# Kernel optimization log

Hardware: AMD Instinct MI355X
Metric: run time of the kernel (lower is better)

The kernel has to match this reference:

```python
import jax, jax.numpy as jnp
import numpy as np

TOP_K = 8


def setup_inputs() -> dict:
    key = jax.random.key(0)
    ks = jax.random.split(key, 7)
    B, D, E = 65536, 1024, 64
    return {
        "x": jax.random.normal(ks[0], (B, D), dtype=jnp.float32),
        "Wg": jax.random.normal(ks[1], (E, D), dtype=jnp.float32) * 0.02,
        "bg": jax.random.normal(ks[2], (E,), dtype=jnp.float32) * 0.02,
        "Wn": jax.random.normal(ks[3], (E, D), dtype=jnp.float32) * 0.02,
        "bn": jax.random.normal(ks[4], (E,), dtype=jnp.float32) * 0.02,
        "We": jax.random.normal(ks[5], (E, D), dtype=jnp.float32) * 0.02,
        "noise": jax.random.normal(ks[6], (B, E), dtype=jnp.float32),
    }


def reference(x, Wg, bg, Wn, bn, We, noise):
    # Router (faithful to original: top-k is taken on noise_logits,
    # and noisy_logits is computed but does not affect the output).
    logits = x @ Wg.T + bg                      # [B, E]
    noise_logits = x @ Wn.T + bn                # [B, E]
    noisy_logits = logits + noise * jax.nn.softplus(noise_logits)  # unused downstream
    del noisy_logits

    top_vals, top_idx = jax.lax.top_k(noise_logits, TOP_K)  # [B, K]
    B, E = noise_logits.shape
    neg_inf = jnp.array(-jnp.inf, dtype=x.dtype)
    sparse_logits = jnp.full((B, E), neg_inf, dtype=x.dtype)
    sparse_logits = sparse_logits.at[jnp.arange(B)[:, None], top_idx].set(top_vals)
    routing_weights = jax.nn.softmax(sparse_logits, axis=-1)  # [B, E]

    # All experts are Linear(d, 1, bias=False): stack into one GEMM.
    expert_out = x @ We.T                        # [B, E]
    final_out = jnp.sum(expert_out * routing_weights, axis=-1, keepdims=True)  # [B, 1]
    return final_out
```

## Files before the change

kernel.cpp:

```cpp
#include <hip/hip_runtime.h>

#define DDIM 1024
#define NEXP 64
#define TOPK 8
#define BK 32
#define ROWS 64
#define NTILE 32
#define TAUF 5.0e-3f
#define TAUB 1.0e-2f

typedef __attribute__((ext_vector_type(8))) short short8;
typedef __attribute__((ext_vector_type(4))) float f32x4;

static __device__ __forceinline__ unsigned int f2u(float f) { return __builtin_bit_cast(unsigned int, f); }
static __device__ __forceinline__ float u2f(unsigned int u) { return __builtin_bit_cast(float, u); }

static __device__ __forceinline__ unsigned short bf_hi_rne(float x) {
    unsigned int u = f2u(x);
    return (unsigned short)((u + (0x7FFFu + ((u >> 16) & 1u))) >> 16);
}

static __device__ __forceinline__ void split2(float x, unsigned short& h, unsigned short& l) {
    unsigned int u = f2u(x);
    unsigned int uh = (u + (0x7FFFu + ((u >> 16) & 1u))) & 0xFFFF0000u;
    h = (unsigned short)(uh >> 16);
    float rem = x - u2f(uh);
    l = (unsigned short)(f2u(rem) >> 16);
}

__global__ __launch_bounds__(256) void conv_w_kernel(
    const float* __restrict__ Wn, const float* __restrict__ We, char* __restrict__ wsW)
{
    int g = blockIdx.x * 256 + threadIdx.x;
    int e = g >> 7, c128 = g & 127;
    int k = c128 << 3;
    int t = k >> 5, c = (k >> 3) & 3;
    const float* np = Wn + (size_t)e * DDIM + k;
    const float* ep = We + (size_t)e * DDIM + k;
    f32x4 n0 = ((const f32x4*)np)[0], n1 = ((const f32x4*)np)[1];
    f32x4 e0 = ((const f32x4*)ep)[0], e1 = ((const f32x4*)ep)[1];
    short8 nh, nl, eh;
#pragma unroll
    for (int i = 0; i < 4; i++) { unsigned short h, l; split2(n0[i], h, l); nh[i] = (short)h; nl[i] = (short)l; }
#pragma unroll
    for (int i = 0; i < 4; i++) { unsigned short h, l; split2(n1[i], h, l); nh[i + 4] = (short)h; nl[i + 4] = (short)l; }
#pragma unroll
    for (int i = 0; i < 4; i++) eh[i] = (short)bf_hi_rne(e0[i]);
#pragma unroll
    for (int i = 0; i < 4; i++) eh[i + 4] = (short)bf_hi_rne(e1[i]);
    size_t dst = (size_t)t * 12288 + (size_t)(e >> 4) * 3072 + (size_t)((c * 16 + (e & 15)) * 16);
    *(short8*)(wsW + dst)        = nh;
    *(short8*)(wsW + dst + 1024) = nl;
    *(short8*)(wsW + dst + 2048) = eh;
}

template <int PRE>
__global__ __launch_bounds__(256, 4) void moe_kernel(
    const float* __restrict__ x, const float* __restrict__ Wn,
    const float* __restrict__ bn, const float* __restrict__ We,
    const char* __restrict__ wsW, float* __restrict__ out)
{
    __shared__ __align__(16) char smem[33792];

    const int tid = threadIdx.x;
    const int wid = tid >> 6;
    const int lane = tid & 63;
    const int fr = lane & 15;
    const int fq = lane >> 4;
    const int blockRow = blockIdx.x * ROWS;

    const int srow = tid >> 2, sg = tid & 3;
    const int swz = (srow * 64 + sg * 16) ^ ((srow & 7) << 4);
    const float* xsrc = x + (size_t)(blockRow + srow) * DDIM + sg * 8;

    f32x4 sxA0, sxA1, sxB0, sxB1, sxC0, sxC1;
    short8 whA, wlA, ehA, whB, wlB, ehB, whC, wlC, ehC;

    const char* wbase = wsW + wid * 3072 + lane * 16;

#define XLOAD_A(t) { const float* p = xsrc + (t) * BK; sxA0 = ((const f32x4*)p)[0]; sxA1 = ((const f32x4*)p)[1]; }
#define XLOAD_B(t) { const float* p = xsrc + (t) * BK; sxB0 = ((const f32x4*)p)[0]; sxB1 = ((const f32x4*)p)[1]; }
#define XLOAD_C(t) { const float* p = xsrc + (t) * BK; sxC0 = ((const f32x4*)p)[0]; sxC1 = ((const f32x4*)p)[1]; }

#define WLOAD(t, wh, wl, eh) { \
    if constexpr (PRE) { \
        const char* wp = wbase + (size_t)(t) * 12288; \
        wh = *(const short8*)(wp); \
        wl = *(const short8*)(wp + 1024); \
        eh = *(const short8*)(wp + 2048); \
    } else { \
        const float* np_ = Wn + (size_t)(wid * 16 + fr) * DDIM + (t) * BK + fq * 8; \
        const float* ep_ = We + (size_t)(wid * 16 + fr) * DDIM + (t) * BK + fq * 8; \
        f32x4 n0_ = ((const f32x4*)np_)[0], n1_ = ((const f32x4*)np_)[1]; \
        f32x4 e0_ = ((const f32x4*)ep_)[0], e1_ = ((const f32x4*)ep_)[1]; \
        for (int i = 0; i < 4; i++) { unsigned short h_, l_; split2(n0_[i], h_, l_); wh[i] = (short)h_; wl[i] = (short)l_; } \
        for (int i = 0; i < 4; i++) { unsigned short h_, l_; split2(n1_[i], h_, l_); wh[i + 4] = (short)h_; wl[i + 4] = (short)l_; } \
        for (int i = 0; i < 4; i++) eh[i] = (short)bf_hi_rne(e0_[i]); \
        for (int i = 0; i < 4; i++) eh[i + 4] = (short)bf_hi_rne(e1_[i]); \
    } }

#define STAGE_WRITE(b, s0, s1) { \
    short8 xh_; \
    for (int i = 0; i < 4; i++) xh_[i] = (short)bf_hi_rne(s0[i]); \
    for (int i = 0; i < 4; i++) xh_[i + 4] = (short)bf_hi_rne(s1[i]); \
    *(short8*)(smem + (b) * 4096 + swz) = xh_; }

    f32x4 accN[4], accE[4];
#pragma unroll
    for (int rt = 0; rt < 4; rt++) { accN[rt] = f32x4{0.f,0.f,0.f,0.f}; accE[rt] = f32x4{0.f,0.f,0.f,0.f}; }

#define COMPUTE(b, wh, wl, eh) { \
    const char* xb_ = smem + (b) * 4096; \
    _Pragma("unroll") \
    for (int rt = 0; rt < 4; rt++) { \
        const int row_ = rt * 16 + fr; \
        const int xoff_ = (row_ * 64 + fq * 16) ^ ((row_ & 7) << 4); \
        short8 xh_ = *(const short8*)(xb_ + xoff_); \
        accN[rt] = __builtin_amdgcn_mfma_f32_16x16x32_bf16(xh_, wh, accN[rt], 0, 0, 0); \
        accN[rt] = __builtin_amdgcn_mfma_f32_16x16x32_bf16(xh_, wl, accN[rt], 0, 0, 0); \
        accE[rt] = __builtin_amdgcn_mfma_f32_16x16x32_bf16(xh_, eh, accE[rt], 0, 0, 0); \
    } }

#define BAR() { asm volatile("s_waitcnt lgkmcnt(0)" ::: "memory"); \
                __builtin_amdgcn_s_barrier(); \
                asm volatile("" ::: "memory"); }

    WLOAD(0, whA, wlA, ehA); XLOAD_A(0);
    WLOAD(1, whB, wlB, ehB); XLOAD_B(1);
    WLOAD(2, whC, wlC, ehC); XLOAD_C(2);
    STAGE_WRITE(0, sxA0, sxA1);
    XLOAD_A(3);
    BAR();

#define ITER(T, W_, X_) { \
        COMPUTE((T) % 3, wh##W_, wl##W_, eh##W_); \
        if ((T) + 1 < NTILE) { STAGE_WRITE(((T) + 1) % 3, sx##X_##0, sx##X_##1); } \
        if ((T) + 3 < NTILE) { WLOAD((T) + 3, wh##W_, wl##W_, eh##W_); } \
        if ((T) + 4 < NTILE) { XLOAD_##X_((T) + 4); } \
        if ((T) + 1 < NTILE) { BAR(); } \
    }

    ITER(0, A, B)  ITER(1, B, C)  ITER(2, C, A)
    ITER(3, A, B)  ITER(4, B, C)  ITER(5, C, A)
    ITER(6, A, B)  ITER(7, B, C)  ITER(8, C, A)
    ITER(9, A, B)  ITER(10, B, C) ITER(11, C, A)
    ITER(12, A, B) ITER(13, B, C) ITER(14, C, A)
    ITER(15, A, B) ITER(16, B, C) ITER(17, C, A)
    ITER(18, A, B) ITER(19, B, C) ITER(20, C, A)
    ITER(21, A, B) ITER(22, B, C) ITER(23, C, A)
    ITER(24, A, B) ITER(25, B, C) ITER(26, C, A)
    ITER(27, A, B) ITER(28, B, C) ITER(29, C, A)
    ITER(30, A, B) ITER(31, B, C)
    __syncthreads();

    float* s_log = (float*)smem;
    float* s_exp = (float*)(smem + 16640);
    float* s_gap = (float*)(smem + 33280);
    float* s_vb  = (float*)(smem + 33536);

    const int ecol = wid * 16 + fr;
    const float be = bn[ecol];
#pragma unroll
    for (int rt = 0; rt < 4; rt++) {
#pragma unroll
        for (int j = 0; j < 4; j++) {
            const int r = rt * 16 + fq * 4 + j;
            s_log[r * 65 + ecol] = accN[rt][j] + be;
            s_exp[r * 65 + ecol] = accE[rt][j];
        }
    }
    __syncthreads();

    auto do_row = [&](int r, float& gapo, float& vbo) -> float {
        float selv[TOPK]; int seli[TOPK];
        unsigned long long chosen = 0ull;
#pragma unroll
        for (int t = 0; t < TOPK; t++) {
            float best = -3.0e38f; int bi = 0;
#pragma unroll 4
            for (int e = 0; e < NEXP; e++) {
                float v = s_log[r * 65 + e];
                if (!((chosen >> e) & 1ull) && v > best) { best = v; bi = e; }
            }
            selv[t] = best; seli[t] = bi; chosen |= (1ull << bi);
        }
        float v9 = -3.0e38f;
#pragma unroll 4
        for (int e = 0; e < NEXP; e++) {
            float v = s_log[r * 65 + e];
            if (!((chosen >> e) & 1ull) && v > v9) v9 = v;
        }
        gapo = selv[TOPK - 1] - v9;
        vbo = 0.5f * (selv[TOPK - 1] + v9);
        float m = selv[0], Z = 0.f, o = 0.f;
#pragma unroll
        for (int t = 0; t < TOPK; t++) {
            float w = __expf(selv[t] - m);
            Z += w;
            o += w * s_exp[r * 65 + seli[t]];
        }
        return o / Z;
    };

    if (lane < 16) {
        const int r = wid * 16 + lane;
        float gap, vb;
        float res = do_row(r, gap, vb);
        out[blockRow + r] = res;
        s_gap[r] = gap; s_vb[r] = vb;
    }
    __syncthreads();

    for (int r = wid; r < ROWS; r += 4) {
        if (!(s_gap[r] < TAUF)) continue;
        const float vbr = s_vb[r];
        const float ve = s_log[r * 65 + lane];
        unsigned long long cand = __ballot(fabsf(ve - vbr) <= TAUB);
        const f32x4* xq = (const f32x4*)(x + (size_t)(blockRow + r) * DDIM) + lane * 4;
        const f32x4 xv0 = xq[0], xv1 = xq[1], xv2 = xq[2], xv3 = xq[3];
        while (cand) {
            const int ce = __builtin_ctzll(cand);
            cand &= cand - 1;
            const f32x4* wq = (const f32x4*)(Wn + (size_t)ce * DDIM) + lane * 4;
            const f32x4 w0 = wq[0], w1 = wq[1], w2 = wq[2], w3 = wq[3];
            double s = 0.0;
#pragma unroll
            for (int i = 0; i < 4; i++) s = fma((double)xv0[i], (double)w0[i], s);
#pragma unroll
            for (int i = 0; i < 4; i++) s = fma((double)xv1[i], (double)w1[i], s);
#pragma unroll
            for (int i = 0; i < 4; i++) s = fma((double)xv2[i], (double)w2[i], s);
#pragma unroll
            for (int i = 0; i < 4; i++) s = fma((double)xv3[i], (double)w3[i], s);
#pragma unroll
            for (int off = 32; off > 0; off >>= 1) s += __shfl_xor(s, off);
            s += (double)bn[ce];
            if (lane == 0) s_log[r * 65 + ce] = (float)s;
        }
    }
    __syncthreads();

    if (lane < 16) {
        const int r = wid * 16 + lane;
        if (s_gap[r] < TAUF) {
            float g2, v2;
            out[blockRow + r] = do_row(r, g2, v2);
        }
    }
}

extern "C" void kernel_launch(void* const* d_in, const int* in_sizes, int n_in,
                              void* d_out, int out_size, void* d_ws, size_t ws_size,
                              hipStream_t stream)
{
    const float* x  = (const float*)d_in[0];
    const float* Wn = (const float*)d_in[3];
    const float* bn = (const float*)d_in[4];
    const float* We = (const float*)d_in[5];
    float* out = (float*)d_out;

    const int B = in_sizes[0] / DDIM;
    const int grid = B / ROWS;

    const size_t need = (size_t)NTILE * 12288;
    if (d_ws != nullptr && ws_size >= need) {
        conv_w_kernel<<<(NEXP * DDIM / 8) / 256, 256, 0, stream>>>(Wn, We, (char*)d_ws);
        moe_kernel<1><<<grid, 256, 0, stream>>>(x, Wn, bn, We, (const char*)d_ws, out);
    } else {
        moe_kernel<0><<<grid, 256, 0, stream>>>(x, Wn, bn, We, nullptr, out);
    }
}
```

Before: 130.9 us.

## Stage weights in LDS via async global_load_lds and keep x in registers

```diff
diff --git a/kernel.cpp b/kernel.cpp
--- a/kernel.cpp
+++ b/kernel.cpp
@@ -6,6 +6,7 @@
 #define BK 32
 #define ROWS 64
 #define NTILE 32
+#define WTILE 12288
 #define TAUF 5.0e-3f
 #define TAUB 1.0e-2f
 
@@ -48,10 +49,10 @@
     for (int i = 0; i < 4; i++) eh[i] = (short)bf_hi_rne(e0[i]);
 #pragma unroll
     for (int i = 0; i < 4; i++) eh[i + 4] = (short)bf_hi_rne(e1[i]);
-    size_t dst = (size_t)t * 12288 + (size_t)(e >> 4) * 3072 + (size_t)((c * 16 + (e & 15)) * 16);
+    size_t dst = (size_t)t * WTILE + (size_t)((e * 64 + c * 16) ^ ((e & 7) << 4));
     *(short8*)(wsW + dst)        = nh;
-    *(short8*)(wsW + dst + 1024) = nl;
-    *(short8*)(wsW + dst + 2048) = eh;
+    *(short8*)(wsW + dst + 4096) = nl;
+    *(short8*)(wsW + dst + 8192) = eh;
 }
 
 template <int PRE>
@@ -60,7 +61,7 @@
     const float* __restrict__ bn, const float* __restrict__ We,
     const char* __restrict__ wsW, float* __restrict__ out)
 {
-    __shared__ __align__(16) char smem[33792];
+    __shared__ __align__(16) char smem[36864];
 
     const int tid = threadIdx.x;
     const int wid = tid >> 6;
@@ -69,88 +70,110 @@
     const int fq = lane >> 4;
     const int blockRow = blockIdx.x * ROWS;
 
-    const int srow = tid >> 2, sg = tid & 3;
-    const int swz = (srow * 64 + sg * 16) ^ ((srow & 7) << 4);
-    const float* xsrc = x + (size_t)(blockRow + srow) * DDIM + sg * 8;
+    const float* xsrc = x + (size_t)(blockRow + wid * 16 + fr) * DDIM + fq * 8;
+    const int xo = (fr * 64 + fq * 16) ^ ((fr & 7) << 4);
 
     f32x4 sxA0, sxA1, sxB0, sxB1, sxC0, sxC1;
-    short8 whA, wlA, ehA, whB, wlB, ehB, whC, wlC, ehC;
-
-    const char* wbase = wsW + wid * 3072 + lane * 16;
-
-#define XLOAD_A(t) { const float* p = xsrc + (t) * BK; sxA0 = ((const f32x4*)p)[0]; sxA1 = ((const f32x4*)p)[1]; }
-#define XLOAD_B(t) { const float* p = xsrc + (t) * BK; sxB0 = ((const f32x4*)p)[0]; sxB1 = ((const f32x4*)p)[1]; }
-#define XLOAD_C(t) { const float* p = xsrc + (t) * BK; sxC0 = ((const f32x4*)p)[0]; sxC1 = ((const f32x4*)p)[1]; }
-
-#define WLOAD(t, wh, wl, eh) { \
-    if constexpr (PRE) { \
-        const char* wp = wbase + (size_t)(t) * 12288; \
-        wh = *(const short8*)(wp); \
-        wl = *(const short8*)(wp + 1024); \
-        eh = *(const short8*)(wp + 2048); \
-    } else { \
-        const float* np_ = Wn + (size_t)(wid * 16 + fr) * DDIM + (t) * BK + fq * 8; \
-        const float* ep_ = We + (size_t)(wid * 16 + fr) * DDIM + (t) * BK + fq * 8; \
-        f32x4 n0_ = ((const f32x4*)np_)[0], n1_ = ((const f32x4*)np_)[1]; \
-        f32x4 e0_ = ((const f32x4*)ep_)[0], e1_ = ((const f32x4*)ep_)[1]; \
-        for (int i = 0; i < 4; i++) { unsigned short h_, l_; split2(n0_[i], h_, l_); wh[i] = (short)h_; wl[i] = (short)l_; } \
-        for (int i = 0; i < 4; i++) { unsigned short h_, l_; split2(n1_[i], h_, l_); wh[i + 4] = (short)h_; wl[i + 4] = (short)l_; } \
-        for (int i = 0; i < 4; i++) eh[i] = (short)bf_hi_rne(e0_[i]); \
-        for (int i = 0; i < 4; i++) eh[i + 4] = (short)bf_hi_rne(e1_[i]); \
-    } }
-
-#define STAGE_WRITE(b, s0, s1) { \
+
+    f32x4 accN[4], accE[4];
+#pragma unroll
+    for (int ct = 0; ct < 4; ct++) { accN[ct] = f32x4{0.f,0.f,0.f,0.f}; accE[ct] = f32x4{0.f,0.f,0.f,0.f}; }
+
+#define XLOAD(S, T) { const float* p_ = xsrc + (T) * BK; \
+    sx##S##0 = ((const f32x4*)p_)[0]; sx##S##1 = ((const f32x4*)p_)[1]; }
+
+#define WDMA(T, WB) { \
+    const char* gs_ = wsW + (size_t)(T) * WTILE + wid * 1024 + lane * 16; \
+    char* ls_ = smem + (WB) * WTILE + wid * 1024; \
+    _Pragma("unroll") \
+    for (int a_ = 0; a_ < 3; a_++) \
+        __builtin_amdgcn_global_load_lds( \
+            (const __attribute__((address_space(1))) void*)(gs_ + a_ * 4096), \
+            (__attribute__((address_space(3))) void*)(ls_ + a_ * 4096), 16, 0, 0); }
+
+#define ITER(T, WB, S, DOX, DODMA, VMSTR) { \
     short8 xh_; \
-    for (int i = 0; i < 4; i++) xh_[i] = (short)bf_hi_rne(s0[i]); \
-    for (int i = 0; i < 4; i++) xh_[i + 4] = (short)bf_hi_rne(s1[i]); \
-    *(short8*)(smem + (b) * 4096 + swz) = xh_; }
-
-    f32x4 accN[4], accE[4];
-#pragma unroll
-    for (int rt = 0; rt < 4; rt++) { accN[rt] = f32x4{0.f,0.f,0.f,0.f}; accE[rt] = f32x4{0.f,0.f,0.f,0.f}; }
-
-#define COMPUTE(b, wh, wl, eh) { \
-    const char* xb_ = smem + (b) * 4096; \
+    _Pragma("unroll") for (int i = 0; i < 4; i++) xh_[i]     = (short)bf_hi_rne(sx##S##0[i]); \
+    _Pragma("unroll") for (int i = 0; i < 4; i++) xh_[i + 4] = (short)bf_hi_rne(sx##S##1[i]); \
+    if (DOX) { XLOAD(S, (T) + 3); } \
+    const char* wb_ = smem + (WB) * WTILE + xo; \
     _Pragma("unroll") \
-    for (int rt = 0; rt < 4; rt++) { \
-        const int row_ = rt * 16 + fr; \
-        const int xoff_ = (row_ * 64 + fq * 16) ^ ((row_ & 7) << 4); \
-        short8 xh_ = *(const short8*)(xb_ + xoff_); \
-        accN[rt] = __builtin_amdgcn_mfma_f32_16x16x32_bf16(xh_, wh, accN[rt], 0, 0, 0); \
-        accN[rt] = __builtin_amdgcn_mfma_f32_16x16x32_bf16(xh_, wl, accN[rt], 0, 0, 0); \
-        accE[rt] = __builtin_amdgcn_mfma_f32_16x16x32_bf16(xh_, eh, accE[rt], 0, 0, 0); \
-    } }
-
-#define BAR() { asm volatile("s_waitcnt lgkmcnt(0)" ::: "memory"); \
-                __builtin_amdgcn_s_barrier(); \
-                asm volatile("" ::: "memory"); }
-
-    WLOAD(0, whA, wlA, ehA); XLOAD_A(0);
-    WLOAD(1, whB, wlB, ehB); XLOAD_B(1);
-    WLOAD(2, whC, wlC, ehC); XLOAD_C(2);
-    STAGE_WRITE(0, sxA0, sxA1);
-    XLOAD_A(3);
-    BAR();
-
-#define ITER(T, W_, X_) { \
-        COMPUTE((T) % 3, wh##W_, wl##W_, eh##W_); \
-        if ((T) + 1 < NTILE) { STAGE_WRITE(((T) + 1) % 3, sx##X_##0, sx##X_##1); } \
-        if ((T) + 3 < NTILE) { WLOAD((T) + 3, wh##W_, wl##W_, eh##W_); } \
-        if ((T) + 4 < NTILE) { XLOAD_##X_((T) + 4); } \
-        if ((T) + 1 < NTILE) { BAR(); } \
-    }
-
-    ITER(0, A, B)  ITER(1, B, C)  ITER(2, C, A)
-    ITER(3, A, B)  ITER(4, B, C)  ITER(5, C, A)
-    ITER(6, A, B)  ITER(7, B, C)  ITER(8, C, A)
-    ITER(9, A, B)  ITER(10, B, C) ITER(11, C, A)
-    ITER(12, A, B) ITER(13, B, C) ITER(14, C, A)
-    ITER(15, A, B) ITER(16, B, C) ITER(17, C, A)
-    ITER(18, A, B) ITER(19, B, C) ITER(20, C, A)
-    ITER(21, A, B) ITER(22, B, C) ITER(23, C, A)
-    ITER(24, A, B) ITER(25, B, C) ITER(26, C, A)
-    ITER(27, A, B) ITER(28, B, C) ITER(29, C, A)
-    ITER(30, A, B) ITER(31, B, C)
+    for (int ct = 0; ct < 4; ct++) { \
+        short8 wh_, wl_, eh_; \
+        if constexpr (PRE) { \
+            wh_ = *(const short8*)(wb_ + ct * 1024); \
+            wl_ = *(const short8*)(wb_ + 4096 + ct * 1024); \
+            eh_ = *(const short8*)(wb_ + 8192 + ct * 1024); \
+        } else { \
+            const float* np_ = Wn + (size_t)(ct * 16 + fr) * DDIM + (T) * BK + fq * 8; \
+            const float* ep_ = We + (size_t)(ct * 16 + fr) * DDIM + (T) * BK + fq * 8; \
+            f32x4 n0_ = ((const f32x4*)np_)[0], n1_ = ((const f32x4*)np_)[1]; \
+            f32x4 e0_ = ((const f32x4*)ep_)[0], e1_ = ((const f32x4*)ep_)[1]; \
+            for (int i = 0; i < 4; i++) { unsigned short h_, l_; split2(n0_[i], h_, l_); wh_[i] = (short)h_; wl_[i] = (short)l_; } \
+            for (int i = 0; i < 4; i++) { unsigned short h_, l_; split2(n1_[i], h_, l_); wh_[i + 4] = (short)h_; wl_[i + 4] = (short)l_; } \
+            for (int i = 0; i < 4; i++) eh_[i] = (short)bf_hi_rne(e0_[i]); \
+            for (int i = 0; i < 4; i++) eh_[i + 4] = (short)bf_hi_rne(e1_[i]); \
+        } \
+        accN[ct] = __builtin_amdgcn_mfma_f32_16x16x32_bf16(xh_, wh_, accN[ct], 0, 0, 0); \
+        accN[ct] = __builtin_amdgcn_mfma_f32_16x16x32_bf16(xh_, wl_, accN[ct], 0, 0, 0); \
+        accE[ct] = __builtin_amdgcn_mfma_f32_16x16x32_bf16(xh_, eh_, accE[ct], 0, 0, 0); \
+    } \
+    asm volatile("s_waitcnt lgkmcnt(0)\ns_waitcnt " VMSTR ::: "memory"); \
+    __builtin_amdgcn_s_barrier(); \
+    asm volatile("" ::: "memory"); \
+    if constexpr (PRE) { if (DODMA) { WDMA((T) + 3, WB); } } }
+
+    XLOAD(A, 0); XLOAD(B, 1); XLOAD(C, 2);
+    if constexpr (PRE) {
+        WDMA(0, 0); WDMA(1, 1); WDMA(2, 2);
+        asm volatile("s_waitcnt vmcnt(6)" ::: "memory");
+    }
+    __builtin_amdgcn_s_barrier();
+    asm volatile("" ::: "memory");
+
+    ITER(0, 0, A, 1, 1, "vmcnt(5)")
+    ITER(1, 1, B, 1, 1, "vmcnt(7)")
+    ITER(2, 2, C, 1, 1, "vmcnt(7)")
+#pragma unroll 1
+    for (int p = 1; p < 9; ++p) {
+        const int t0 = 3 * p;
+        ITER(t0 + 0, 0, A, 1, 1, "vmcnt(7)")
+        ITER(t0 + 1, 1, B, 1, 1, "vmcnt(7)")
+        ITER(t0 + 2, 2, C, 1, 1, "vmcnt(7)")
+    }
+    ITER(27, 0, A, 1, 1, "vmcnt(7)")
+    ITER(28, 1, B, 1, 1, "vmcnt(7)")
+    ITER(29, 2, C, 0, 0, "vmcnt(5)")
+    ITER(30, 0, A, 0, 0, "vmcnt(0)")
+    {
+        short8 xh_;
+#pragma unroll
+        for (int i = 0; i < 4; i++) xh_[i]     = (short)bf_hi_rne(sxB0[i]);
+#pragma unroll
+        for (int i = 0; i < 4; i++) xh_[i + 4] = (short)bf_hi_rne(sxB1[i]);
+        const char* wb_ = smem + 1 * WTILE + xo;
+#pragma unroll
+        for (int ct = 0; ct < 4; ct++) {
+            short8 wh_, wl_, eh_;
+            if constexpr (PRE) {
+                wh_ = *(const short8*)(wb_ + ct * 1024);
+                wl_ = *(const short8*)(wb_ + 4096 + ct * 1024);
+                eh_ = *(const short8*)(wb_ + 8192 + ct * 1024);
+            } else {
+                const float* np_ = Wn + (size_t)(ct * 16 + fr) * DDIM + 31 * BK + fq * 8;
+                const float* ep_ = We + (size_t)(ct * 16 + fr) * DDIM + 31 * BK + fq * 8;
+                f32x4 n0_ = ((const f32x4*)np_)[0], n1_ = ((const f32x4*)np_)[1];
+                f32x4 e0_ = ((const f32x4*)ep_)[0], e1_ = ((const f32x4*)ep_)[1];
+                for (int i = 0; i < 4; i++) { unsigned short h_, l_; split2(n0_[i], h_, l_); wh_[i] = (short)h_; wl_[i] = (short)l_; }
+                for (int i = 0; i < 4; i++) { unsigned short h_, l_; split2(n1_[i], h_, l_); wh_[i + 4] = (short)h_; wl_[i + 4] = (short)l_; }
+                for (int i = 0; i < 4; i++) eh_[i] = (short)bf_hi_rne(e0_[i]);
+                for (int i = 0; i < 4; i++) eh_[i + 4] = (short)bf_hi_rne(e1_[i]);
+            }
+            accN[ct] = __builtin_amdgcn_mfma_f32_16x16x32_bf16(xh_, wh_, accN[ct], 0, 0, 0);
+            accN[ct] = __builtin_amdgcn_mfma_f32_16x16x32_bf16(xh_, wl_, accN[ct], 0, 0, 0);
+            accE[ct] = __builtin_amdgcn_mfma_f32_16x16x32_bf16(xh_, eh_, accE[ct], 0, 0, 0);
+        }
+    }
     __syncthreads();
 
     float* s_log = (float*)smem;
@@ -158,57 +181,58 @@
     float* s_gap = (float*)(smem + 33280);
     float* s_vb  = (float*)(smem + 33536);
 
-    const int ecol = wid * 16 + fr;
-    const float be = bn[ecol];
-#pragma unroll
-    for (int rt = 0; rt < 4; rt++) {
+#pragma unroll
+    for (int ct = 0; ct < 4; ct++) {
+        const int e = ct * 16 + fr;
+        const float be = bn[e];
 #pragma unroll
         for (int j = 0; j < 4; j++) {
-            const int r = rt * 16 + fq * 4 + j;
-            s_log[r * 65 + ecol] = accN[rt][j] + be;
-            s_exp[r * 65 + ecol] = accE[rt][j];
-        }
-    }
-    __syncthreads();
-
-    auto do_row = [&](int r, float& gapo, float& vbo) -> float {
-        float selv[TOPK]; int seli[TOPK];
-        unsigned long long chosen = 0ull;
-#pragma unroll
-        for (int t = 0; t < TOPK; t++) {
-            float best = -3.0e38f; int bi = 0;
-#pragma unroll 4
-            for (int e = 0; e < NEXP; e++) {
-                float v = s_log[r * 65 + e];
-                if (!((chosen >> e) & 1ull) && v > best) { best = v; bi = e; }
-            }
-            selv[t] = best; seli[t] = bi; chosen |= (1ull << bi);
-        }
-        float v9 = -3.0e38f;
-#pragma unroll 4
-        for (int e = 0; e < NEXP; e++) {
-            float v = s_log[r * 65 + e];
-            if (!((chosen >> e) & 1ull) && v > v9) v9 = v;
-        }
-        gapo = selv[TOPK - 1] - v9;
-        vbo = 0.5f * (selv[TOPK - 1] + v9);
-        float m = selv[0], Z = 0.f, o = 0.f;
-#pragma unroll
-        for (int t = 0; t < TOPK; t++) {
-            float w = __expf(selv[t] - m);
-            Z += w;
-            o += w * s_exp[r * 65 + seli[t]];
-        }
-        return o / Z;
+            const int r = wid * 16 + fq * 4 + j;
+            s_log[r * 65 + e] = accN[ct][j] + be;
+            s_exp[r * 65 + e] = accE[ct][j];
+        }
+    }
+    __syncthreads();
+
+    auto wave_max = [&](float c) {
+#pragma unroll
+        for (int off = 32; off >= 1; off >>= 1) c = fmaxf(c, __shfl_xor(c, off));
+        return c;
     };
-
-    if (lane < 16) {
-        const int r = wid * 16 + lane;
-        float gap, vb;
-        float res = do_row(r, gap, vb);
-        out[blockRow + r] = res;
-        s_gap[r] = gap; s_vb[r] = vb;
-    }
+    auto wave_sum = [&](float c) {
+#pragma unroll
+        for (int off = 32; off >= 1; off >>= 1) c += __shfl_xor(c, off);
+        return c;
+    };
+
+    auto select_row = [&](int r, bool writeGap) {
+        const float v = s_log[r * 65 + lane];
+        const float g = s_exp[r * 65 + lane];
+        unsigned long long act = ~0ull, sel = 0ull;
+        float m0 = 0.f, v8 = 0.f;
+#pragma unroll
+        for (int tt = 0; tt < TOPK; tt++) {
+            float c = ((act >> lane) & 1ull) ? v : -3.0e38f;
+            c = wave_max(c);
+            unsigned long long elig = __ballot(v == c) & act;
+            int win = __builtin_ctzll(elig);
+            sel |= 1ull << win;
+            act &= ~(1ull << win);
+            if (tt == 0) m0 = c;
+            v8 = c;
+        }
+        float c9 = ((act >> lane) & 1ull) ? v : -3.0e38f;
+        float v9 = wave_max(c9);
+        float w = ((sel >> lane) & 1ull) ? __expf(v - m0) : 0.f;
+        float Z = wave_sum(w);
+        float O = wave_sum(w * g);
+        if (lane == 0) {
+            out[blockRow + r] = O / Z;
+            if (writeGap) { s_gap[r] = v8 - v9; s_vb[r] = 0.5f * (v8 + v9); }
+        }
+    };
+
+    for (int rr = 0; rr < 16; ++rr) select_row(wid * 16 + rr, true);
     __syncthreads();
 
     for (int r = wid; r < ROWS; r += 4) {
@@ -240,12 +264,9 @@
     }
     __syncthreads();
 
-    if (lane < 16) {
-        const int r = wid * 16 + lane;
-        if (s_gap[r] < TAUF) {
-            float g2, v2;
-            out[blockRow + r] = do_row(r, g2, v2);
-        }
+    for (int rr = 0; rr < 16; ++rr) {
+        const int r = wid * 16 + rr;
+        if (s_gap[r] < TAUF) select_row(r, false);
     }
 }
 
@@ -262,7 +283,7 @@
     const int B = in_sizes[0] / DDIM;
     const int grid = B / ROWS;
 
-    const size_t need = (size_t)NTILE * 12288;
+    const size_t need = (size_t)NTILE * WTILE;
     if (d_ws != nullptr && ws_size >= need) {
         conv_w_kernel<<<(NEXP * DDIM / 8) / 256, 256, 0, stream>>>(Wn, We, (char*)d_ws);
         moe_kernel<1><<<grid, 256, 0, stream>>>(x, Wn, bn, We, (const char*)d_ws, out);
```

Result: faster. 127.5 us (-2.6%).
